# Kernel optimization log

Hardware: AMD Instinct MI355X
Metric: run time of the kernel (lower is better)

The kernel has to match this reference:

```python
import jax, jax.numpy as jnp
import numpy as np

B, N, H = 8, 512, 256
D2 = H // 2          # per-direction hidden = attention proj = 128
VOCAB, EMB = 100, 256
DIN0 = EMB + 3


def _sru_pp_layer(x, pad, Wq, Wk, Wv, Wu, vf, vr, bf, br):
    # x: (L, Bt, din); pad: (L, Bt) bool, True = padded position
    L, Bt, _ = x.shape
    d2 = Wu.shape[1] // 8
    q = x @ Wq                                   # (L,Bt,proj) attention projection
    k = q @ Wk
    v = q @ Wv
    scale = 1.0 / jnp.sqrt(jnp.asarray(q.shape[-1], q.dtype))
    scores = jnp.einsum('lbp,mbp->blm', q, k) * scale
    scores = jnp.where(pad.T[:, None, :], -1e9, scores)
    a = jnp.einsum('blm,mbp->lbp', jax.nn.softmax(scores, axis=-1), v) + q
    U = (a @ Wu).reshape(L, Bt, 2, 4, d2)        # 2 directions x 4 matrices

    def run_dir(Ud, padd, vf_d, vr_d, bf_d, br_d):
        def step(c, inp):
            u, p = inp                            # u: (Bt,4,d2), p: (Bt,)
            f = jax.nn.sigmoid(u[:, 1] + vf_d * c + bf_d)
            r = jax.nn.sigmoid(u[:, 2] + vr_d * c + br_d)
            c_new = f * c + (1.0 - f) * u[:, 0]
            c_new = jnp.where(p[:, None], c, c_new)
            h = jnp.where(p[:, None], 0.0, r * c_new + (1.0 - r) * u[:, 3])
            return c_new, h
        c0 = jnp.zeros((Bt, d2), x.dtype)
        _, hs = jax.lax.scan(step, c0, (Ud, padd))
        return hs

    hf = run_dir(U[:, :, 0], pad, vf[0], vr[0], bf[0], br[0])
    hb = run_dir(U[::-1, :, 1], pad[::-1], vf[1], vr[1], bf[1], br[1])[::-1]
    return jnp.concatenate([hf, hb], axis=-1)     # (L,Bt,2*d2)


def _forward(noisy_seqs, noisy_cords, mask, emb, params):
    Bb, Nn = noisy_seqs.shape
    X = noisy_cords[:, :, 1]                      # CA coordinates (B,N,3)
    m3 = mask[..., None]
    center = (X * m3).sum(1) / m3.sum(1)
    Xc = X - center[:, None] * m3
    C = jnp.einsum('bni,bnj->bij', Xc, Xc)        # (B,3,3) covariance
    _, V = jnp.linalg.eigh(jax.lax.stop_gradient(C))
    ops = jnp.asarray([[i, j, k] for i in (-1, 1) for j in (-1, 1) for k in (-1, 1)], X.dtype)
    F_ops = ops[None, :, None, :] * V[:, None]    # (B,8,3,3) sign-flipped frames
    hX = jnp.einsum('boji,bpj->bopi', F_ops, Xc).reshape(Bb * 8, Nn, 3)
    seq = jnp.where(noisy_seqs < 0, 82, noisy_seqs)
    hS = jnp.broadcast_to(emb[seq][:, None], (Bb, 8, Nn, emb.shape[1])).reshape(Bb * 8, Nn, -1)
    h = jnp.swapaxes(jnp.concatenate([hX, hS], -1), 0, 1)   # (N, B*8, EMB+3)
    pad = jnp.broadcast_to((mask == 0.0)[:, None], (Bb, 8, Nn)).reshape(Bb * 8, Nn).T
    for p in params:
        h = _sru_pp_layer(h, pad, *p)
    return jnp.swapaxes(h, 0, 1).reshape(Bb, 8, Nn, -1).mean(1)


def setup_inputs():
    key = jax.random.key(0)
    ks = [jax.random.fold_in(key, i) for i in range(32)]
    inp = {
        'noisy_seqs': jax.random.randint(ks[0], (B, N), 0, VOCAB, dtype=jnp.int32),
        'noisy_cords': jax.random.normal(ks[1], (B, N, 4, 3), jnp.float32),
        'mask': jnp.ones((B, N), jnp.float32),
        'emb': 0.02 * jax.random.normal(ks[2], (VOCAB, EMB), jnp.float32),
    }
    i = 3
    for l, din in enumerate([DIN0, H]):
        inp[f'Wq{l}'] = jax.random.normal(ks[i], (din, D2), jnp.float32) / np.sqrt(din); i += 1
        inp[f'Wk{l}'] = jax.random.normal(ks[i], (D2, D2), jnp.float32) / np.sqrt(D2); i += 1
        inp[f'Wv{l}'] = jax.random.normal(ks[i], (D2, D2), jnp.float32) / np.sqrt(D2); i += 1
        inp[f'Wu{l}'] = jax.random.normal(ks[i], (D2, 8 * D2), jnp.float32) / np.sqrt(D2); i += 1
        inp[f'vf{l}'] = 0.1 * jax.random.normal(ks[i], (2, D2), jnp.float32); i += 1
        inp[f'vr{l}'] = 0.1 * jax.random.normal(ks[i], (2, D2), jnp.float32); i += 1
        inp[f'bf{l}'] = jnp.zeros((2, D2), jnp.float32)
        inp[f'br{l}'] = jnp.zeros((2, D2), jnp.float32)
    return inp


def reference(noisy_seqs, noisy_cords, mask, emb,
              Wq0, Wk0, Wv0, Wu0, vf0, vr0, bf0, br0,
              Wq1, Wk1, Wv1, Wu1, vf1, vr1, bf1, br1):
    params = [(Wq0, Wk0, Wv0, Wu0, vf0, vr0, bf0, br0),
              (Wq1, Wk1, Wv1, Wu1, vf1, vr1, bf1, br1)]
    return _forward(noisy_seqs, noisy_cords, mask, emb, params)
```

## Files before the change

kernel.cpp:

```cpp
#include <hip/hip_runtime.h>
#include <hip/hip_bf16.h>
#include <math.h>

#define L_    512
#define F_    64
#define M_    (F_*L_)
#define D2_   128
#define H_    256
#define LOG2E_ 1.4426950408889634f

typedef unsigned short u16;
typedef __attribute__((ext_vector_type(8))) short s16x8;
typedef __attribute__((ext_vector_type(4))) float f32x4;

__device__ inline u16 bf_hi(float x) {
  union { float f; unsigned u; } v; v.f = x;
  unsigned r = v.u + 0x7fffu + ((v.u >> 16) & 1u);
  return (u16)(r >> 16);
}
__device__ inline float bf_to_f(u16 h) {
  union { float f; unsigned u; } v; v.u = ((unsigned)h) << 16; return v.f;
}
__device__ inline void split2(float x, u16& h, u16& l) {
  h = bf_hi(x);
  l = bf_hi(x - bf_to_f(h));
}
__device__ inline float exp2_fast(float x) {
#if __has_builtin(__builtin_amdgcn_exp2f)
  return __builtin_amdgcn_exp2f(x);
#else
  return __expf(x * 0.6931471805599453f);
#endif
}
__device__ inline float rcp_fast(float x) {
#if __has_builtin(__builtin_amdgcn_rcpf)
  return __builtin_amdgcn_rcpf(x);
#else
  return 1.f/x;
#endif
}

#define RSPLIT_A 18432
#define RSPLIT_B 26624

__global__ void geom_kernel(const float* __restrict__ cords, const float* __restrict__ mask,
                            float* __restrict__ misc) {
  int b = blockIdx.x;
  int t = threadIdx.x;
  __shared__ float red[4][256];
  float sx=0.f, sy=0.f, sz=0.f, sm=0.f;
  for (int l = t; l < 512; l += 256) {
    float m = mask[b*512 + l];
    const float* X = cords + ((size_t)(b*512 + l)*4 + 1)*3;
    sx += X[0]*m; sy += X[1]*m; sz += X[2]*m; sm += m;
  }
  red[0][t]=sx; red[1][t]=sy; red[2][t]=sz; red[3][t]=sm;
  __syncthreads();
  for (int off=128; off>0; off>>=1) {
    if (t < off) { red[0][t]+=red[0][t+off]; red[1][t]+=red[1][t+off];
                   red[2][t]+=red[2][t+off]; red[3][t]+=red[3][t+off]; }
    __syncthreads();
  }
  float inv = 1.f/red[3][0];
  float cx = red[0][0]*inv, cy = red[1][0]*inv, cz = red[2][0]*inv;
  __syncthreads();
  __shared__ float red6[6][256];
  float c00=0,c01=0,c02=0,c11=0,c12=0,c22=0;
  for (int l = t; l < 512; l += 256) {
    float m = mask[b*512+l];
    const float* X = cords + ((size_t)(b*512+l)*4 + 1)*3;
    float x = X[0]-cx*m, y = X[1]-cy*m, z = X[2]-cz*m;
    c00+=x*x; c01+=x*y; c02+=x*z; c11+=y*y; c12+=y*z; c22+=z*z;
  }
  red6[0][t]=c00; red6[1][t]=c01; red6[2][t]=c02;
  red6[3][t]=c11; red6[4][t]=c12; red6[5][t]=c22;
  __syncthreads();
  for (int off=128; off>0; off>>=1) {
    if (t < off) for (int j=0;j<6;j++) red6[j][t]+=red6[j][t+off];
    __syncthreads();
  }
  if (t == 0) {
    double A[3][3], V[3][3];
    A[0][0]=red6[0][0]; A[0][1]=A[1][0]=red6[1][0]; A[0][2]=A[2][0]=red6[2][0];
    A[1][1]=red6[3][0]; A[1][2]=A[2][1]=red6[4][0]; A[2][2]=red6[5][0];
    for (int j=0;j<3;j++) for (int i=0;i<3;i++) V[j][i] = (i==j)?1.0:0.0;
    for (int sweep=0; sweep<10; ++sweep) {
      for (int p=0;p<2;p++) for (int q=p+1;q<3;q++) {
        double apq = A[p][q];
        if (fabs(apq) < 1e-18) continue;
        double app = A[p][p], aqq = A[q][q];
        double tau = (aqq - app) / (2.0*apq);
        double tt = (tau >= 0.0) ? 1.0/(tau + sqrt(1.0+tau*tau))
                                 : 1.0/(tau - sqrt(1.0+tau*tau));
        double cc = 1.0/sqrt(1.0+tt*tt), ss = tt*cc;
        A[p][p] = app - tt*apq;
        A[q][q] = aqq + tt*apq;
        A[p][q] = A[q][p] = 0.0;
        int r = 3 - p - q;
        double arp = A[r][p], arq = A[r][q];
        A[r][p] = A[p][r] = cc*arp - ss*arq;
        A[r][q] = A[q][r] = ss*arp + cc*arq;
        for (int rr2=0; rr2<3; ++rr2) {
          double vrp = V[rr2][p], vrq = V[rr2][q];
          V[rr2][p] = cc*vrp - ss*vrq;
          V[rr2][q] = ss*vrp + cc*vrq;
        }
      }
    }
    double w[3] = {A[0][0], A[1][1], A[2][2]};
    int idx[3] = {0,1,2};
    for (int i=0;i<2;i++) for (int j=0;j<2-i;j++)
      if (w[idx[j]] > w[idx[j+1]]) { int tmp=idx[j]; idx[j]=idx[j+1]; idx[j+1]=tmp; }
    for (int jj=0;jj<3;jj++) for (int ii=0;ii<3;ii++)
      misc[b*12 + jj*3 + ii] = (float)V[jj][idx[ii]];
    misc[b*12+9]=cx; misc[b*12+10]=cy; misc[b*12+11]=cz;
  }
}

__global__ void build_h0(const int* __restrict__ seqs, const float* __restrict__ cords,
                         const float* __restrict__ mask, const float* __restrict__ emb,
                         const float* __restrict__ misc,
                         u16* __restrict__ h0h, u16* __restrict__ h0l) {
  int t = threadIdx.x;
  int r = blockIdx.x*4 + (t >> 6);
  int lane = t & 63;
  int f = r >> 9, l = r & 511;
  int b = f >> 3, o = f & 7;
  u16* rh = h0h + (size_t)r * 288;
  u16* rl = h0l + (size_t)r * 288;
  if (lane == 0) {
    float m = mask[b*512 + l];
    const float* X = cords + ((size_t)(b*512 + l)*4 + 1)*3;
    const float* mb = misc + b*12;
    float x = X[0]-mb[9]*m, y = X[1]-mb[10]*m, z = X[2]-mb[11]*m;
    #pragma unroll
    for (int i=0;i<3;i++) {
      float sgn = ((o >> (2-i)) & 1) ? 1.f : -1.f;
      float val = sgn * (mb[0+i]*x + mb[3+i]*y + mb[6+i]*z);
      u16 h,lo; split2(val,h,lo); rh[i]=h; rl[i]=lo;
    }
  }
  if (lane < 29) { rh[259+lane] = 0; rl[259+lane] = 0; }
  int s = seqs[b*512 + l];
  if (s < 0) s = 82;
  const float4 e4 = *((const float4*)(emb + (size_t)s*256) + lane);
  float ev[4] = {e4.x, e4.y, e4.z, e4.w};
  #pragma unroll
  for (int i=0;i<4;i++) {
    u16 h,lo; split2(ev[i],h,lo);
    rh[3 + lane*4 + i] = h; rl[3 + lane*4 + i] = lo;
  }
}

__global__ void prep_wqkv_mul(const float* __restrict__ Wq, const float* __restrict__ Wk,
                              const float* __restrict__ Wv,
                              float* __restrict__ wqk, float* __restrict__ wqv) {
  int k = blockIdx.x;
  int y = blockIdx.y;
  int t = threadIdx.x;
  __shared__ float row[128];
  row[t] = Wq[(size_t)k*128 + t];
  __syncthreads();
  const float* W2 = y ? Wv : Wk;
  float acc = 0.f;
  for (int j = 0; j < 128; j++) acc += row[j] * W2[(size_t)j*128 + t];
  (y ? wqv : wqk)[(size_t)k*128 + t] = acc;
}

__global__ void prep_wT3(const float* __restrict__ Wq, const float* __restrict__ wqk,
                         const float* __restrict__ wqv,
                         u16* __restrict__ Th, u16* __restrict__ Tl,
                         int K, int KP) {
  int y = blockIdx.y;
  int n = blockIdx.x;
  const float* W = (y==0) ? Wq : (y==1) ? wqk : wqv;
  int row = y*128 + n;
  for (int k = threadIdx.x; k < KP; k += 128) {
    float x = (k < K) ? W[(size_t)k*128 + n] : 0.f;
    u16 h,l; split2(x,h,l);
    Th[(size_t)row*KP + k] = h; Tl[(size_t)row*KP + k] = l;
  }
}

__global__ void prep_wu(const float* __restrict__ Wu, u16* __restrict__ Th, u16* __restrict__ Tl,
                        const float* __restrict__ bfv, const float* __restrict__ brv,
                        float* __restrict__ nbf, float* __restrict__ nbr) {
  int n = blockIdx.x;
  int dir = blockIdx.y;
  int k = threadIdx.x;
  int d = n >> 2, g = n & 3;
  float x = Wu[(size_t)k*1024 + (dir*4+g)*128 + d];
  if (g == 1 || g == 2) x *= -LOG2E_;
  u16 h,l; split2(x,h,l);
  size_t o = ((size_t)dir*512 + n)*128 + k;
  Th[o]=h; Tl[o]=l;
  if (n == 0) {
    nbf[dir*128 + k] = bfv[dir*128 + k] * (-LOG2E_);
    nbr[dir*128 + k] = brv[dir*128 + k] * (-LOG2E_);
  }
}

template<int EPI>
__global__ __launch_bounds__(256) void gemm_bb(
    const u16* __restrict__ Ah, const u16* __restrict__ Al,
    const u16* __restrict__ Bh, const u16* __restrict__ Bl,
    int KP, int lda, int ldb,
    long aBatch, long bBatch, long cBatch,
    u16* __restrict__ Ch, u16* __restrict__ Cl, int ldc,
    u16* __restrict__ Dh, u16* __restrict__ Dl,
    u16* __restrict__ Eh, u16* __restrict__ El,
    float* __restrict__ F0, float* __restrict__ F1, float* __restrict__ F2,
    float* __restrict__ F3, float* __restrict__ F4, float* __restrict__ F5,
    const u16* __restrict__ rh, const u16* __restrict__ rl,
    const float* __restrict__ maskp, const float* __restrict__ nbf,
    const float* __restrict__ nbr, float scale, int dirOff)
{
  __shared__ u16 As[2][128][40];
  __shared__ u16 Bs[2][128][40];
  __shared__ float epsM[128];
  __shared__ float epsA[128];
  const int t = threadIdx.x;
  const int z = blockIdx.z;
  const int bm = blockIdx.x * 128, bn = blockIdx.y * 128;
  Ah += (size_t)z * aBatch; Al += (size_t)z * aBatch;
  Bh += (size_t)z * bBatch; Bl += (size_t)z * bBatch;

  const int lane = t & 63;
  const int w = t >> 6, wr = w >> 1, wc = w & 1;
  const int fr = lane & 15, g = lane >> 4;

  const bool isD1 = (bn >= 512);
  const int dirU = dirOff + (isD1 ? 1 : 0);
  if (EPI == 4) {
    if (t < 128) {
      int r = bm + t;
      epsM[t] = maskp[(r >> 12)*512 + (r & 511)];
      int nl = (bn + t) & 511;
      int dd = nl >> 2, gg2 = nl & 3;
      epsA[t] = (gg2==1) ? nbf[dirU*128 + dd] : (gg2==2) ? nbr[dirU*128 + dd] : 0.f;
    }
  }

  f32x4 acc[4][4] = {};

  for (int k0 = 0; k0 < KP; k0 += 32) {
    #pragma unroll
    for (int cc = 0; cc < 2; cc++) {
      int c = t + cc*256;
      int m = c >> 2, sub = c & 3;
      const size_t ga = (size_t)(bm + m)*lda + k0 + sub*8;
      const size_t gb = (size_t)(bn + m)*ldb + k0 + sub*8;
      *(int4*)&As[0][m][sub*8] = *(const int4*)(Ah + ga);
      *(int4*)&As[1][m][sub*8] = *(const int4*)(Al + ga);
      *(int4*)&Bs[0][m][sub*8] = *(const int4*)(Bh + gb);
      *(int4*)&Bs[1][m][sub*8] = *(const int4*)(Bl + gb);
    }
    __syncthreads();
    s16x8 af[4][2], bfr[4][2];
    #pragma unroll
    for (int i = 0; i < 4; i++) {
      af[i][0]  = *(const s16x8*)&As[0][wr*64 + i*16 + fr][g*8];
      af[i][1]  = *(const s16x8*)&As[1][wr*64 + i*16 + fr][g*8];
      bfr[i][0] = *(const s16x8*)&Bs[0][wc*64 + i*16 + fr][g*8];
      bfr[i][1] = *(const s16x8*)&Bs[1][wc*64 + i*16 + fr][g*8];
    }
    #pragma unroll
    for (int mi = 0; mi < 4; mi++)
      #pragma unroll
      for (int nj = 0; nj < 4; nj++)
        acc[mi][nj] = __builtin_amdgcn_mfma_f32_16x16x32_bf16(af[mi][0], bfr[nj][0], acc[mi][nj], 0,0,0);
    #pragma unroll
    for (int mi = 0; mi < 4; mi++)
      #pragma unroll
      for (int nj = 0; nj < 4; nj++)
        acc[mi][nj] = __builtin_amdgcn_mfma_f32_16x16x32_bf16(af[mi][0], bfr[nj][1], acc[mi][nj], 0,0,0);
    #pragma unroll
    for (int mi = 0; mi < 4; mi++)
      #pragma unroll
      for (int nj = 0; nj < 4; nj++)
        acc[mi][nj] = __builtin_amdgcn_mfma_f32_16x16x32_bf16(af[mi][1], bfr[nj][0], acc[mi][nj], 0,0,0);
    __syncthreads();
  }

  const int rbase = bm + wr*64, nbase = bn + wc*64;
  float* tA = isD1 ? F3 : F0;
  float* tB = isD1 ? F4 : F1;
  float* tC = isD1 ? F5 : F2;
  const int gg = fr & 3;
  const float ovr = (gg==1) ? -16384.f : (gg==2) ? 16384.f : 0.f;

  #pragma unroll
  for (int mi = 0; mi < 4; mi++) {
    #pragma unroll
    for (int nj = 0; nj < 4; nj++) {
      #pragma unroll
      for (int rg = 0; rg < 4; rg++) {
        int r = rbase + mi*16 + g*4 + rg;
        int n = nbase + nj*16 + fr;
        float val = acc[mi][nj][rg];
        if (EPI == 2) {
          float vv = val * scale;
          if (maskp[(z>>3)*512 + n] == 0.f) vv = -1e9f;
          F0[(size_t)z*cBatch + (size_t)r*ldc + n] = vv;
        } else if (EPI == 3) {
          size_t o = (size_t)z*cBatch + (size_t)r*ldc + n;
          float vv = val + (bf_to_f(rh[o]) + bf_to_f(rl[o]));
          u16 h,l; split2(vv,h,l);
          Ch[o]=h; Cl[o]=l;
        } else if (EPI == 4) {
          int nloc = (n & 511);
          val += epsA[n - bn];
          if (epsM[r - bm] == 0.f) val = ovr;
          float* Up;
          if (r < RSPLIT_A)      Up = tA + (size_t)r*512;
          else if (r < RSPLIT_B) Up = tB + (size_t)(r - RSPLIT_A)*512;
          else                   Up = tC + (size_t)(r - RSPLIT_B)*512;
          Up[nloc] = val;
        } else {
          u16 h,l; split2(val,h,l);
          if (blockIdx.y == 0) {
            size_t o = (size_t)r*128 + n;
            Ch[o]=h; Cl[o]=l;
          } else if (blockIdx.y == 1) {
            size_t o = (size_t)r*128 + (n - 128);
            Dh[o]=h; Dl[o]=l;
          } else {
            size_t o = ((size_t)(r >> 9)*128 + (n - 256))*512 + (r & 511);
            Eh[o]=h; El[o]=l;
          }
        }
      }
    }
  }
}

__global__ __launch_bounds__(256) void attn_flash(
    const u16* __restrict__ qh, const u16* __restrict__ ql,
    const u16* __restrict__ kh, const u16* __restrict__ kl,
    const u16* __restrict__ vTh, const u16* __restrict__ vTl,
    const float* __restrict__ maskp,
    u16* __restrict__ ah, u16* __restrict__ al, float scale)
{
  __shared__ u16 As[2][64][36];
  __shared__ u16 Bs[2][128][36];
  __shared__ u16 Ps[2][64][68];
  __shared__ float rmaxL[2][64];
  __shared__ float rsumL[2][64];
  __shared__ float mskt[64];
  const int t = threadIdx.x;
  const int f = blockIdx.y;
  const int bq = f >> 3;
  const int bm = blockIdx.x * 64;
  const size_t qrow0 = (size_t)f*512 + bm;
  const int lane = t & 63;
  const int w = t >> 6, wr = w >> 1, wc = w & 1;
  const int fr = lane & 15, g = lane >> 4;
  const int m_ = t >> 2, sub_ = t & 3;

  float mrun[2][4], srun[2][4];
  #pragma unroll
  for (int mi=0;mi<2;mi++)
    #pragma unroll
    for (int rg=0;rg<4;rg++) { mrun[mi][rg] = -3e38f; srun[mi][rg] = 0.f; }
  f32x4 Oacc[2][4] = {};

  for (int kt = 0; kt < 8; ++kt) {
    if (t < 64) mskt[t] = maskp[bq*512 + kt*64 + t];
    f32x4 Sacc[2][2] = {};
    #pragma unroll
    for (int k0 = 0; k0 < 4; ++k0) {
      {
        const size_t ga = (qrow0 + m_)*128 + k0*32 + sub_*8;
        const size_t gb = ((size_t)f*512 + kt*64 + m_)*128 + k0*32 + sub_*8;
        *(int4*)&As[0][m_][sub_*8] = *(const int4*)(qh + ga);
        *(int4*)&As[1][m_][sub_*8] = *(const int4*)(ql + ga);
        *(int4*)&Bs[0][m_][sub_*8] = *(const int4*)(kh + gb);
        *(int4*)&Bs[1][m_][sub_*8] = *(const int4*)(kl + gb);
      }
      __syncthreads();
      s16x8 af[2][2], bf2[2][2];
      #pragma unroll
      for (int i = 0; i < 2; i++) {
        af[i][0]  = *(const s16x8*)&As[0][wr*32 + i*16 + fr][g*8];
        af[i][1]  = *(const s16x8*)&As[1][wr*32 + i*16 + fr][g*8];
        bf2[i][0] = *(const s16x8*)&Bs[0][wc*32 + i*16 + fr][g*8];
        bf2[i][1] = *(const s16x8*)&Bs[1][wc*32 + i*16 + fr][g*8];
      }
      #pragma unroll
      for (int mi = 0; mi < 2; mi++)
        #pragma unroll
        for (int nj = 0; nj < 2; nj++)
          Sacc[mi][nj] = __builtin_amdgcn_mfma_f32_16x16x32_bf16(af[mi][0], bf2[nj][0], Sacc[mi][nj], 0,0,0);
      #pragma unroll
      for (int mi = 0; mi < 2; mi++)
        #pragma unroll
        for (int nj = 0; nj < 2; nj++)
          Sacc[mi][nj] = __builtin_amdgcn_mfma_f32_16x16x32_bf16(af[mi][0], bf2[nj][1], Sacc[mi][nj], 0,0,0);
      #pragma unroll
      for (int mi = 0; mi < 2; mi++)
        #pragma unroll
        for (int nj = 0; nj < 2; nj++)
          Sacc[mi][nj] = __builtin_amdgcn_mfma_f32_16x16x32_bf16(af[mi][1], bf2[nj][0], Sacc[mi][nj], 0,0,0);
      __syncthreads();
    }
    float mkv[2];
    mkv[0] = mskt[wc*32 + fr];
    mkv[1] = mskt[wc*32 + 16 + fr];
    float rm[2][4];
    #pragma unroll
    for (int mi=0;mi<2;mi++)
      #pragma unroll
      for (int rg=0;rg<4;rg++) rm[mi][rg] = -3e38f;
    #pragma unroll
    for (int mi=0;mi<2;mi++)
      #pragma unroll
      for (int nj=0;nj<2;nj++)
        #pragma unroll
        for (int rg=0;rg<4;rg++) {
          float sv = Sacc[mi][nj][rg]*scale;
          sv = (mkv[nj]==0.f) ? -1e9f : sv;
          Sacc[mi][nj][rg] = sv;
          rm[mi][rg] = fmaxf(rm[mi][rg], sv);
        }
    #pragma unroll
    for (int off=1; off<16; off<<=1)
      #pragma unroll
      for (int mi=0;mi<2;mi++)
        #pragma unroll
        for (int rg=0;rg<4;rg++) rm[mi][rg] = fmaxf(rm[mi][rg], __shfl_xor(rm[mi][rg], off));
    if (fr == 0) {
      #pragma unroll
      for (int mi=0;mi<2;mi++)
        #pragma unroll
        for (int rg=0;rg<4;rg++) rmaxL[wc][wr*32 + mi*16 + g*4 + rg] = rm[mi][rg];
    }
    __syncthreads();
    float alpha[2][4], rs[2][4];
    #pragma unroll
    for (int mi=0;mi<2;mi++)
      #pragma unroll
      for (int rg=0;rg<4;rg++) {
        int rl_ = wr*32 + mi*16 + g*4 + rg;
        float tmax = fmaxf(rmaxL[0][rl_], rmaxL[1][rl_]);
        float mn = fmaxf(mrun[mi][rg], tmax);
        alpha[mi][rg] = exp2_fast((mrun[mi][rg] - mn)*LOG2E_);
        mrun[mi][rg] = mn;
        rs[mi][rg] = 0.f;
      }
    #pragma unroll
    for (int mi=0;mi<2;mi++)
      #pragma unroll
      for (int nj=0;nj<2;nj++)
        #pragma unroll
        for (int rg=0;rg<4;rg++) {
          float p = exp2_fast((Sacc[mi][nj][rg] - mrun[mi][rg])*LOG2E_);
          rs[mi][rg] += p;
          u16 h,l; split2(p,h,l);
          int rl_ = wr*32 + mi*16 + g*4 + rg;
          int cl_ = wc*32 + nj*16 + fr;
          Ps[0][rl_][cl_] = h;
          Ps[1][rl_][cl_] = l;
        }
    #pragma unroll
    for (int off=1; off<16; off<<=1)
      #pragma unroll
      for (int mi=0;mi<2;mi++)
        #pragma unroll
        for (int rg=0;rg<4;rg++) rs[mi][rg] += __shfl_xor(rs[mi][rg], off);
    if (fr == 0) {
      #pragma unroll
      for (int mi=0;mi<2;mi++)
        #pragma unroll
        for (int rg=0;rg<4;rg++) rsumL[wc][wr*32 + mi*16 + g*4 + rg] = rs[mi][rg];
    }
    #pragma unroll
    for (int mi=0;mi<2;mi++)
      #pragma unroll
      for (int nj=0;nj<4;nj++)
        #pragma unroll
        for (int rg=0;rg<4;rg++) Oacc[mi][nj][rg] *= alpha[mi][rg];
    __syncthreads();
    #pragma unroll
    for (int mi=0;mi<2;mi++)
      #pragma unroll
      for (int rg=0;rg<4;rg++) {
        int rl_ = wr*32 + mi*16 + g*4 + rg;
        srun[mi][rg] = srun[mi][rg]*alpha[mi][rg] + rsumL[0][rl_] + rsumL[1][rl_];
      }
    #pragma unroll
    for (int k0 = 0; k0 < 2; ++k0) {
      #pragma unroll
      for (int cc = 0; cc < 2; cc++) {
        int c = t + cc*256;
        int mv = c >> 2, sb = c & 3;
        const size_t gv = ((size_t)f*128 + mv)*512 + kt*64 + k0*32 + sb*8;
        *(int4*)&Bs[0][mv][sb*8] = *(const int4*)(vTh + gv);
        *(int4*)&Bs[1][mv][sb*8] = *(const int4*)(vTl + gv);
      }
      __syncthreads();
      s16x8 pa[2][2], pb[4][2];
      #pragma unroll
      for (int i = 0; i < 2; i++) {
        pa[i][0] = *(const s16x8*)&Ps[0][wr*32 + i*16 + fr][k0*32 + g*8];
        pa[i][1] = *(const s16x8*)&Ps[1][wr*32 + i*16 + fr][k0*32 + g*8];
      }
      #pragma unroll
      for (int j = 0; j < 4; j++) {
        pb[j][0] = *(const s16x8*)&Bs[0][wc*64 + j*16 + fr][g*8];
        pb[j][1] = *(const s16x8*)&Bs[1][wc*64 + j*16 + fr][g*8];
      }
      #pragma unroll
      for (int mi = 0; mi < 2; mi++)
        #pragma unroll
        for (int nj = 0; nj < 4; nj++)
          Oacc[mi][nj] = __builtin_amdgcn_mfma_f32_16x16x32_bf16(pa[mi][0], pb[nj][0], Oacc[mi][nj], 0,0,0);
      #pragma unroll
      for (int mi = 0; mi < 2; mi++)
        #pragma unroll
        for (int nj = 0; nj < 4; nj++)
          Oacc[mi][nj] = __builtin_amdgcn_mfma_f32_16x16x32_bf16(pa[mi][0], pb[nj][1], Oacc[mi][nj], 0,0,0);
      #pragma unroll
      for (int mi = 0; mi < 2; mi++)
        #pragma unroll
        for (int nj = 0; nj < 4; nj++)
          Oacc[mi][nj] = __builtin_amdgcn_mfma_f32_16x16x32_bf16(pa[mi][1], pb[nj][0], Oacc[mi][nj], 0,0,0);
      __syncthreads();
    }
  }
  float inv[2][4];
  #pragma unroll
  for (int mi=0;mi<2;mi++)
    #pragma unroll
    for (int rg=0;rg<4;rg++) inv[mi][rg] = 1.f / srun[mi][rg];
  #pragma unroll
  for (int mi=0;mi<2;mi++)
    #pragma unroll
    for (int nj=0;nj<4;nj++)
      #pragma unroll
      for (int rg=0;rg<4;rg++) {
        int rl_ = wr*32 + mi*16 + g*4 + rg;
        int cl_ = wc*64 + nj*16 + fr;
        size_t o = (qrow0 + rl_)*128 + cl_;
        float val = Oacc[mi][nj][rg]*inv[mi][rg] + bf_to_f(qh[o]) + bf_to_f(ql[o]);
        u16 h,l; split2(val,h,l);
        ah[o]=h; al[o]=l;
      }
}

__global__ void softmax_split(float* __restrict__ S) {
  size_t row = blockIdx.x;
  float* p = S + row*512;
  u16* ph = (u16*)p;
  u16* pl = ph + 512;
  int t = threadIdx.x;
  float v[8];
  float mx = -1e30f;
  #pragma unroll
  for (int i=0;i<8;i++) { v[i] = p[t + i*64]; mx = fmaxf(mx, v[i]); }
  #pragma unroll
  for (int off=32; off>0; off>>=1) mx = fmaxf(mx, __shfl_xor(mx, off));
  float sum = 0.f;
  #pragma unroll
  for (int i=0;i<8;i++) { v[i] = __expf(v[i]-mx); sum += v[i]; }
  #pragma unroll
  for (int off=32; off>0; off>>=1) sum += __shfl_xor(sum, off);
  float invs = 1.f/sum;
  #pragma unroll
  for (int i=0;i<8;i++) {
    float x = v[i]*invs;
    u16 h,l; split2(x,h,l);
    ph[t + i*64] = h; pl[t + i*64] = l;
  }
}

#define CH_ 8
#define LOADC(buf, ch) do { \
  int _c = (ch); \
  _Pragma("unroll") \
  for (int s = 0; s < CH_; s++) { \
    int l = (_c*CH_ + s) ^ lxor; \
    buf[s] = *(const float4*)(Ubase + (size_t)l*512); \
  } \
  __builtin_amdgcn_sched_barrier(0); \
} while(0)

#define COMPC(buf, ch) do { \
  int _c = (ch); \
  _Pragma("unroll") \
  for (int s = 0; s < CH_; s++) { \
    int l = (_c*CH_ + s) ^ lxor; \
    float4 u = buf[s]; \
    float ef = exp2_fast(fmaf(nvfd, cstate, u.y)); \
    float fg = rcp_fast(1.f + ef); \
    float er = exp2_fast(fmaf(nvrd, cstate, u.z)); \
    float rg = rcp_fast(1.f + er); \
    float cn = fmaf(fg, cstate - u.x, u.x); \
    float h  = fmaf(rg, cn - u.w, u.w); \
    cstate = cn; \
    if (PAIRS) { \
      u16 sh_, sl_; split2(h, sh_, sl_); \
      hpph[(size_t)l*256] = sh_; \
      hppl[(size_t)l*256] = sl_; \
    } else { \
      h32p[(size_t)l*256] = h; \
    } \
  } \
  __builtin_amdgcn_sched_barrier(0); \
} while(0)

template<int PAIRS>
__global__ __launch_bounds__(64, 1) void sru_scan(
                          const float* __restrict__ ua0, const float* __restrict__ ub0,
                          const float* __restrict__ uc0,
                          const float* __restrict__ ua1, const float* __restrict__ ub1,
                          const float* __restrict__ uc1,
                          const float* __restrict__ vf, const float* __restrict__ vr,
                          u16* __restrict__ hph, u16* __restrict__ hpl,
                          float* __restrict__ h32, int dirArg) {
  const int blk = blockIdx.x;
  const int f = blk >> 1;
  const int hh = blk & 1;
  const int dir = dirArg + blockIdx.y;
  const int t = threadIdx.x;
  const int lxor = dir ? 511 : 0;
  const int d = hh*64 + t;
  const float nvfd = vf[dir*128 + d] * (-LOG2E_);
  const float nvrd = vr[dir*128 + d] * (-LOG2E_);
  const size_t fbase = (size_t)f * 512;
  const float* ua = dir ? ua1 : ua0;
  const float* ub = dir ? ub1 : ub0;
  const float* uc = dir ? uc1 : uc0;
  const float* Uf;
  if (f < 36)      Uf = ua + (size_t)f*(512*512);
  else if (f < 52) Uf = ub + (size_t)(f-36)*(512*512);
  else             Uf = uc + (size_t)(f-52)*(512*512);
  const float* Ubase = Uf + d*4;
  u16* hpph = hph + fbase*256 + (size_t)dir*128 + d;
  u16* hppl = hpl + fbase*256 + (size_t)dir*128 + d;
  float* h32p = h32 + fbase*256 + (size_t)dir*128 + d;

  float4 b0[CH_], b1[CH_], b2[CH_], b3[CH_];
  LOADC(b0, 0); LOADC(b1, 1);
  float cstate = 0.f;
  #pragma unroll 1
  for (int q4 = 0; q4 < 15; q4++) {
    const int base = q4*4;
    LOADC(b2, base+2);
    COMPC(b0, base);
    LOADC(b3, base+3);
    COMPC(b1, base+1);
    LOADC(b0, base+4);
    COMPC(b2, base+2);
    LOADC(b1, base+5);
    COMPC(b3, base+3);
  }
  LOADC(b2, 62);
  COMPC(b0, 60);
  LOADC(b3, 63);
  COMPC(b1, 61);
  COMPC(b2, 62);
  COMPC(b3, 63);
}

__global__ void mean_kernel(const float* __restrict__ h2, float* __restrict__ out) {
  int i = blockIdx.x*256 + threadIdx.x;
  int row = i >> 6;
  int c4  = i & 63;
  int b = row >> 9, l = row & 511;
  float ax=0.f, ay=0.f, az=0.f, aw=0.f;
  #pragma unroll
  for (int o=0;o<8;o++) {
    const float4* p = (const float4*)(h2 + ((size_t)((b*8+o)*512 + l))*256) + c4;
    float4 e = *p;
    ax += e.x; ay += e.y; az += e.z; aw += e.w;
  }
  float4 r; r.x = ax*0.125f; r.y = ay*0.125f; r.z = az*0.125f; r.w = aw*0.125f;
  ((float4*)out)[i] = r;
}

extern "C" void kernel_launch(void* const* d_in, const int* in_sizes, int n_in,
                              void* d_out, int out_size, void* d_ws, size_t ws_size,
                              hipStream_t stream) {
  const int*   seqs  = (const int*)d_in[0];
  const float* cords = (const float*)d_in[1];
  const float* mask  = (const float*)d_in[2];
  const float* emb   = (const float*)d_in[3];
  const float* Wq[2] = {(const float*)d_in[4],  (const float*)d_in[12]};
  const float* Wk[2] = {(const float*)d_in[5],  (const float*)d_in[13]};
  const float* Wv[2] = {(const float*)d_in[6],  (const float*)d_in[14]};
  const float* Wu[2] = {(const float*)d_in[7],  (const float*)d_in[15]};
  const float* vf[2] = {(const float*)d_in[8],  (const float*)d_in[16]};
  const float* vr[2] = {(const float*)d_in[9],  (const float*)d_in[17]};
  const float* bfp[2]= {(const float*)d_in[10], (const float*)d_in[18]};
  const float* brp[2]= {(const float*)d_in[11], (const float*)d_in[19]};

  const size_t H0_B = 2*(size_t)M_*288*2;
  const size_t Q_B  = 2*(size_t)M_*128*2;
  const size_t S_B  = (size_t)M_*512*4;
  const size_t HP_B = 2*(size_t)M_*256*2;
  const size_t W_B  = (size_t)(2*1024*128)*2 + 2*256*4;

  const size_t NEED_MERGED = 4096 + H0_B + 3*Q_B + S_B + HP_B + W_B;
  const bool merged = (ws_size >= NEED_MERGED);

  char* base = (char*)d_ws;
  float* misc = (float*)base;
  u16* h0p_h = (u16*)(base + 4096);
  u16* h0p_l = h0p_h + (size_t)M_*288;
  u16* q_h   = (u16*)(base + 4096 + H0_B);
  u16* q_l   = q_h + (size_t)M_*128;
  u16* k_h   = (u16*)(base + 4096 + H0_B + Q_B);
  u16* k_l   = k_h + (size_t)M_*128;

  u16 *vT_h, *vT_l, *a_h, *a_l;
  float *S, *tail_w;
  u16 *hp_h, *hp_l;
  float *U1A, *U1B, *U1C;
  if (merged) {
    vT_h = (u16*)(base + 4096 + H0_B + 2*Q_B);
    vT_l = vT_h + (size_t)M_*128;
    S    = (float*)(base + 4096 + H0_B + 3*Q_B);
    hp_h = (u16*)((char*)S + S_B);
    hp_l = hp_h + (size_t)M_*256;
    tail_w = (float*)((char*)hp_h + HP_B);
    U1A = (float*)h0p_h;
    U1B = (float*)q_h;
    U1C = (float*)vT_h;
    a_h = hp_h;
    a_l = hp_h + (size_t)M_*128;
  } else {
    S    = (float*)(base + 4096 + H0_B + 2*Q_B);
    hp_h = (u16*)((char*)S + S_B);
    hp_l = hp_h + (size_t)M_*256;
    vT_h = hp_h; vT_l = hp_l;
    tail_w = (float*)((char*)hp_h + HP_B);
    U1A = S; U1B = S + (size_t)RSPLIT_A*512; U1C = S + (size_t)RSPLIT_B*512;
    a_h = k_h; a_l = k_l;
  }
  float* U0A = S;
  float* U0B = S + (size_t)RSPLIT_A*512;
  float* U0C = S + (size_t)RSPLIT_B*512;
  float* h32 = (float*)hp_h;

  float* wqk32 = S;
  float* wqv32 = wqk32 + 288*128;
  u16*   wT3h  = (u16*)(wqv32 + 288*128);
  u16*   wT3l  = wT3h + 384*288;
  u16* wuT_h = (u16*)tail_w;
  u16* wuT_l = wuT_h + 1024*128;
  float* nbf = (float*)(wuT_l + 1024*128);
  float* nbr = nbf + 256;

  geom_kernel<<<8, 256, 0, stream>>>(cords, mask, misc);
  build_h0<<<M_/4, 256, 0, stream>>>(seqs, cords, mask, emb, misc, h0p_h, h0p_l);

  const float scale = 0.08838834764831845f;
  for (int layer = 0; layer < 2; ++layer) {
    const u16* Ah_in = layer ? hp_h : h0p_h;
    const u16* Al_in = layer ? hp_l : h0p_l;
    const int  Kq    = layer ? 256 : 259;
    const int  KPq   = layer ? 256 : 288;

    prep_wqkv_mul<<<dim3(Kq,2), 128, 0, stream>>>(Wq[layer], Wk[layer], Wv[layer], wqk32, wqv32);
    prep_wT3<<<dim3(128,3), 128, 0, stream>>>(Wq[layer], wqk32, wqv32, wT3h, wT3l, Kq, KPq);
    prep_wu<<<dim3(512,2), 128, 0, stream>>>(Wu[layer], wuT_h, wuT_l, bfp[layer], brp[layer], nbf, nbr);

    gemm_bb<5><<<dim3(256,3,1), 256, 0, stream>>>(Ah_in, Al_in, wT3h, wT3l,
        KPq, KPq, KPq, 0,0,0, q_h, q_l, 128, k_h, k_l, vT_h, vT_l,
        nullptr,nullptr,nullptr,nullptr,nullptr,nullptr,
        nullptr,nullptr, nullptr,nullptr,nullptr, 0.f, 0);

    if (merged) {
      attn_flash<<<dim3(8,64), 256, 0, stream>>>(q_h, q_l, k_h, k_l, vT_h, vT_l,
          mask, a_h, a_l, scale);
    } else {
      gemm_bb<2><<<dim3(4,4,64), 256, 0, stream>>>(q_h, q_l, k_h, k_l,
          128, 128, 128, 512*128, 512*128, 512*512, nullptr,nullptr, 512,
          nullptr,nullptr,nullptr,nullptr,
          S,nullptr,nullptr,nullptr,nullptr,nullptr,
          nullptr,nullptr, mask,nullptr,nullptr, scale, 0);
      softmax_split<<<M_, 64, 0, stream>>>(S);
      gemm_bb<3><<<dim3(4,1,64), 256, 0, stream>>>((const u16*)S, (const u16*)S + 512, vT_h, vT_l,
          512, 1024, 512, 512*1024, 128*512, 512*128, a_h, a_l, 128,
          nullptr,nullptr,nullptr,nullptr,
          nullptr,nullptr,nullptr,nullptr,nullptr,nullptr,
          q_h, q_l, nullptr,nullptr,nullptr, 0.f, 0);
    }

    if (merged) {
      gemm_bb<4><<<dim3(256,8,1), 256, 0, stream>>>(a_h, a_l, wuT_h, wuT_l,
          128, 128, 128, 0,0,0, nullptr,nullptr, 512,
          nullptr,nullptr,nullptr,nullptr,
          U0A,U0B,U0C, U1A,U1B,U1C,
          nullptr,nullptr, mask, nbf, nbr, 0.f, 0);
      if (layer == 0)
        sru_scan<1><<<dim3(128,2), 64, 0, stream>>>(U0A,U0B,U0C, U1A,U1B,U1C,
            vf[layer], vr[layer], hp_h, hp_l, h32, 0);
      else
        sru_scan<0><<<dim3(128,2), 64, 0, stream>>>(U0A,U0B,U0C, U1A,U1B,U1C,
            vf[layer], vr[layer], hp_h, hp_l, h32, 0);
    } else {
      for (int dir = 0; dir < 2; ++dir) {
        gemm_bb<4><<<dim3(256,4,1), 256, 0, stream>>>(a_h, a_l,
            wuT_h + (size_t)dir*512*128, wuT_l + (size_t)dir*512*128,
            128, 128, 128, 0,0,0, nullptr,nullptr, 512,
            nullptr,nullptr,nullptr,nullptr,
            U0A,U0B,U0C, U0A,U0B,U0C,
            nullptr,nullptr, mask, nbf, nbr, 0.f, dir);
        if (layer == 0)
          sru_scan<1><<<dim3(128,1), 64, 0, stream>>>(U0A,U0B,U0C, U0A,U0B,U0C,
              vf[layer], vr[layer], hp_h, hp_l, h32, dir);
        else
          sru_scan<0><<<dim3(128,1), 64, 0, stream>>>(U0A,U0B,U0C, U0A,U0B,U0C,
              vf[layer], vr[layer], hp_h, hp_l, h32, dir);
      }
    }
  }
  mean_kernel<<<1024, 256, 0, stream>>>(h32, (float*)d_out);
}
```

Baseline: 468.4 us.

## Fuse U projection GEMM into SRU scan kernel via LDS-staged chunks

Replaces the separate U-projection GEMM (which wrote the full fp32 U tensor to global memory) and the following SRU scan with a single fused kernel. Each block computes 64-timestep chunks of U for its sequence, direction and channel half with MFMA, stages them in about 120KB of LDS, then one wavefront runs the recurrence over the chunk. This removes the large U global write and read. In exchange only 64 of 256 threads do the serial scan while the others idle, and the grid has just 256 blocks at one block per CU.

```diff
diff --git a/kernel.cpp b/kernel.cpp
--- a/kernel.cpp
+++ b/kernel.cpp
@@ -39,9 +39,6 @@
   return 1.f/x;
 #endif
 }
-
-#define RSPLIT_A 18432
-#define RSPLIT_B 26624
 
 __global__ void geom_kernel(const float* __restrict__ cords, const float* __restrict__ mask,
                             float* __restrict__ misc) {
@@ -209,16 +206,12 @@
     u16* __restrict__ Ch, u16* __restrict__ Cl, int ldc,
     u16* __restrict__ Dh, u16* __restrict__ Dl,
     u16* __restrict__ Eh, u16* __restrict__ El,
-    float* __restrict__ F0, float* __restrict__ F1, float* __restrict__ F2,
-    float* __restrict__ F3, float* __restrict__ F4, float* __restrict__ F5,
+    float* __restrict__ F0,
     const u16* __restrict__ rh, const u16* __restrict__ rl,
-    const float* __restrict__ maskp, const float* __restrict__ nbf,
-    const float* __restrict__ nbr, float scale, int dirOff)
+    const float* __restrict__ maskp, float scale)
 {
   __shared__ u16 As[2][128][40];
   __shared__ u16 Bs[2][128][40];
-  __shared__ float epsM[128];
-  __shared__ float epsA[128];
   const int t = threadIdx.x;
   const int z = blockIdx.z;
   const int bm = blockIdx.x * 128, bn = blockIdx.y * 128;
@@ -228,18 +221,6 @@
   const int lane = t & 63;
   const int w = t >> 6, wr = w >> 1, wc = w & 1;
   const int fr = lane & 15, g = lane >> 4;
-
-  const bool isD1 = (bn >= 512);
-  const int dirU = dirOff + (isD1 ? 1 : 0);
-  if (EPI == 4) {
-    if (t < 128) {
-      int r = bm + t;
-      epsM[t] = maskp[(r >> 12)*512 + (r & 511)];
-      int nl = (bn + t) & 511;
-      int dd = nl >> 2, gg2 = nl & 3;
-      epsA[t] = (gg2==1) ? nbf[dirU*128 + dd] : (gg2==2) ? nbr[dirU*128 + dd] : 0.f;
-    }
-  }
 
   f32x4 acc[4][4] = {};
 
@@ -283,12 +264,6 @@
   }
 
   const int rbase = bm + wr*64, nbase = bn + wc*64;
-  float* tA = isD1 ? F3 : F0;
-  float* tB = isD1 ? F4 : F1;
-  float* tC = isD1 ? F5 : F2;
-  const int gg = fr & 3;
-  const float ovr = (gg==1) ? -16384.f : (gg==2) ? 16384.f : 0.f;
-
   #pragma unroll
   for (int mi = 0; mi < 4; mi++) {
     #pragma unroll
@@ -307,15 +282,6 @@
           float vv = val + (bf_to_f(rh[o]) + bf_to_f(rl[o]));
           u16 h,l; split2(vv,h,l);
           Ch[o]=h; Cl[o]=l;
-        } else if (EPI == 4) {
-          int nloc = (n & 511);
-          val += epsA[n - bn];
-          if (epsM[r - bm] == 0.f) val = ovr;
-          float* Up;
-          if (r < RSPLIT_A)      Up = tA + (size_t)r*512;
-          else if (r < RSPLIT_B) Up = tB + (size_t)(r - RSPLIT_A)*512;
-          else                   Up = tC + (size_t)(r - RSPLIT_B)*512;
-          Up[nloc] = val;
         } else {
           u16 h,l; split2(val,h,l);
           if (blockIdx.y == 0) {
@@ -573,93 +539,138 @@
   }
 }
 
-#define CH_ 8
-#define LOADC(buf, ch) do { \
-  int _c = (ch); \
-  _Pragma("unroll") \
-  for (int s = 0; s < CH_; s++) { \
-    int l = (_c*CH_ + s) ^ lxor; \
-    buf[s] = *(const float4*)(Ubase + (size_t)l*512); \
-  } \
-  __builtin_amdgcn_sched_barrier(0); \
-} while(0)
-
-#define COMPC(buf, ch) do { \
-  int _c = (ch); \
-  _Pragma("unroll") \
-  for (int s = 0; s < CH_; s++) { \
-    int l = (_c*CH_ + s) ^ lxor; \
-    float4 u = buf[s]; \
-    float ef = exp2_fast(fmaf(nvfd, cstate, u.y)); \
-    float fg = rcp_fast(1.f + ef); \
-    float er = exp2_fast(fmaf(nvrd, cstate, u.z)); \
-    float rg = rcp_fast(1.f + er); \
-    float cn = fmaf(fg, cstate - u.x, u.x); \
-    float h  = fmaf(rg, cn - u.w, u.w); \
-    cstate = cn; \
-    if (PAIRS) { \
-      u16 sh_, sl_; split2(h, sh_, sl_); \
-      hpph[(size_t)l*256] = sh_; \
-      hppl[(size_t)l*256] = sl_; \
-    } else { \
-      h32p[(size_t)l*256] = h; \
-    } \
-  } \
-  __builtin_amdgcn_sched_barrier(0); \
-} while(0)
-
+#define SRU_LDS_BYTES 122176
 template<int PAIRS>
-__global__ __launch_bounds__(64, 1) void sru_scan(
-                          const float* __restrict__ ua0, const float* __restrict__ ub0,
-                          const float* __restrict__ uc0,
-                          const float* __restrict__ ua1, const float* __restrict__ ub1,
-                          const float* __restrict__ uc1,
-                          const float* __restrict__ vf, const float* __restrict__ vr,
-                          u16* __restrict__ hph, u16* __restrict__ hpl,
-                          float* __restrict__ h32, int dirArg) {
-  const int blk = blockIdx.x;
-  const int f = blk >> 1;
-  const int hh = blk & 1;
-  const int dir = dirArg + blockIdx.y;
+__global__ __launch_bounds__(256, 1) void sru_fused(
+    const u16* __restrict__ Ah, const u16* __restrict__ Al,
+    const u16* __restrict__ wuTh, const u16* __restrict__ wuTl,
+    const float* __restrict__ maskp,
+    const float* __restrict__ nbf, const float* __restrict__ nbr,
+    const float* __restrict__ vf, const float* __restrict__ vr,
+    u16* __restrict__ hph, u16* __restrict__ hpl, float* __restrict__ h32)
+{
+  extern __shared__ char smem[];
+  float* Uc   = (float*)smem;
+  u16*   As   = (u16*)(smem + 69696);
+  u16*   Bs   = (u16*)(smem + 69696 + 10240);
+  float* epsA = (float*)(smem + 120896);
+  float* mskc = (float*)(smem + 121920);
+  const int UPL = 4356;
+
+  const int f = blockIdx.x, dir = blockIdx.y, hh = blockIdx.z;
   const int t = threadIdx.x;
-  const int lxor = dir ? 511 : 0;
-  const int d = hh*64 + t;
-  const float nvfd = vf[dir*128 + d] * (-LOG2E_);
-  const float nvrd = vr[dir*128 + d] * (-LOG2E_);
-  const size_t fbase = (size_t)f * 512;
-  const float* ua = dir ? ua1 : ua0;
-  const float* ub = dir ? ub1 : ub0;
-  const float* uc = dir ? uc1 : uc0;
-  const float* Uf;
-  if (f < 36)      Uf = ua + (size_t)f*(512*512);
-  else if (f < 52) Uf = ub + (size_t)(f-36)*(512*512);
-  else             Uf = uc + (size_t)(f-52)*(512*512);
-  const float* Ubase = Uf + d*4;
-  u16* hpph = hph + fbase*256 + (size_t)dir*128 + d;
-  u16* hppl = hpl + fbase*256 + (size_t)dir*128 + d;
-  float* h32p = h32 + fbase*256 + (size_t)dir*128 + d;
-
-  float4 b0[CH_], b1[CH_], b2[CH_], b3[CH_];
-  LOADC(b0, 0); LOADC(b1, 1);
+  const int lane = t & 63, w = t >> 6;
+  const int fr = lane & 15, g = lane >> 4;
+  const int b = f >> 3;
+
+  {
+    int gate = t & 3, dl = t >> 2;
+    int ch = dir*128 + hh*64 + dl;
+    epsA[t] = (gate==1) ? nbf[ch] : (gate==2) ? nbr[ch] : 0.f;
+  }
+  const float nvfd = vf[dir*128 + hh*64 + lane] * (-LOG2E_);
+  const float nvrd = vr[dir*128 + hh*64 + lane] * (-LOG2E_);
+  const int chx = dir ? 7 : 0, lx = dir ? 63 : 0;
+  const int gate = fr & 3;
+  const float ovr = (gate==1) ? -16384.f : (gate==2) ? 16384.f : 0.f;
   float cstate = 0.f;
+
   #pragma unroll 1
-  for (int q4 = 0; q4 < 15; q4++) {
-    const int base = q4*4;
-    LOADC(b2, base+2);
-    COMPC(b0, base);
-    LOADC(b3, base+3);
-    COMPC(b1, base+1);
-    LOADC(b0, base+4);
-    COMPC(b2, base+2);
-    LOADC(b1, base+5);
-    COMPC(b3, base+3);
-  }
-  LOADC(b2, 62);
-  COMPC(b0, 60);
-  LOADC(b3, 63);
-  COMPC(b1, 61);
-  COMPC(b2, 62);
-  COMPC(b3, 63);
+  for (int ci = 0; ci < 8; ++ci) {
+    const int ch = ci ^ chx;
+    if (t < 64) mskc[t] = maskp[b*512 + ch*64 + t];
+    f32x4 acc[4][4] = {};
+    #pragma unroll 1
+    for (int k0 = 0; k0 < 4; ++k0) {
+      {
+        int m = t >> 2, sub = t & 3;
+        size_t ga = ((size_t)f*512 + ch*64 + m)*128 + k0*32 + sub*8;
+        *(int4*)&As[(0*64 + m)*40 + sub*8] = *(const int4*)(Ah + ga);
+        *(int4*)&As[(1*64 + m)*40 + sub*8] = *(const int4*)(Al + ga);
+      }
+      {
+        size_t gb = ((size_t)(dir*512 + hh*256 + t))*128 + k0*32;
+        #pragma unroll
+        for (int s4 = 0; s4 < 4; ++s4) {
+          *(int4*)&Bs[(0*256 + t)*40 + s4*8] = *(const int4*)(wuTh + gb + s4*8);
+          *(int4*)&Bs[(1*256 + t)*40 + s4*8] = *(const int4*)(wuTl + gb + s4*8);
+        }
+      }
+      __syncthreads();
+      s16x8 af[4][2], bfr[4][2];
+      #pragma unroll
+      for (int i = 0; i < 4; i++) {
+        af[i][0]  = *(const s16x8*)&As[(0*64 + i*16 + fr)*40 + g*8];
+        af[i][1]  = *(const s16x8*)&As[(1*64 + i*16 + fr)*40 + g*8];
+        bfr[i][0] = *(const s16x8*)&Bs[(0*256 + w*64 + i*16 + fr)*40 + g*8];
+        bfr[i][1] = *(const s16x8*)&Bs[(1*256 + w*64 + i*16 + fr)*40 + g*8];
+      }
+      #pragma unroll
+      for (int mi = 0; mi < 4; mi++)
+        #pragma unroll
+        for (int nj = 0; nj < 4; nj++)
+          acc[mi][nj] = __builtin_amdgcn_mfma_f32_16x16x32_bf16(af[mi][0], bfr[nj][0], acc[mi][nj], 0,0,0);
+      #pragma unroll
+      for (int mi = 0; mi < 4; mi++)
+        #pragma unroll
+        for (int nj = 0; nj < 4; nj++)
+          acc[mi][nj] = __builtin_amdgcn_mfma_f32_16x16x32_bf16(af[mi][0], bfr[nj][1], acc[mi][nj], 0,0,0);
+      #pragma unroll
+      for (int mi = 0; mi < 4; mi++)
+        #pragma unroll
+        for (int nj = 0; nj < 4; nj++)
+          acc[mi][nj] = __builtin_amdgcn_mfma_f32_16x16x32_bf16(af[mi][1], bfr[nj][0], acc[mi][nj], 0,0,0);
+      __syncthreads();
+    }
+    #pragma unroll
+    for (int mi = 0; mi < 4; mi++) {
+      #pragma unroll
+      for (int nj = 0; nj < 4; nj++) {
+        int nl = w*64 + nj*16 + fr;
+        int dl = nl >> 2;
+        float ea = epsA[nl];
+        #pragma unroll
+        for (int rg = 0; rg < 4; rg++) {
+          int r = mi*16 + g*4 + rg;
+          float val = acc[mi][nj][rg] + ea;
+          if (mskc[r] == 0.f) val = ovr;
+          Uc[gate*UPL + r*68 + dl] = val;
+        }
+      }
+    }
+    __syncthreads();
+    if (t < 64) {
+      const int d = t;
+      int l0 = 0 ^ lx, l1 = 1 ^ lx;
+      float a0 = Uc[0*UPL + l0*68 + d], a1 = Uc[1*UPL + l0*68 + d];
+      float a2 = Uc[2*UPL + l0*68 + d], a3 = Uc[3*UPL + l0*68 + d];
+      float b0 = Uc[0*UPL + l1*68 + d], b1 = Uc[1*UPL + l1*68 + d];
+      float b2 = Uc[2*UPL + l1*68 + d], b3 = Uc[3*UPL + l1*68 + d];
+      #pragma unroll 4
+      for (int si = 0; si < 64; ++si) {
+        float n0=0.f, n1=0.f, n2=0.f, n3=0.f;
+        if (si + 2 < 64) {
+          int ln = (si+2) ^ lx;
+          n0 = Uc[0*UPL + ln*68 + d]; n1 = Uc[1*UPL + ln*68 + d];
+          n2 = Uc[2*UPL + ln*68 + d]; n3 = Uc[3*UPL + ln*68 + d];
+        }
+        float ef = exp2_fast(fmaf(nvfd, cstate, a1));
+        float fg = rcp_fast(1.f + ef);
+        float er = exp2_fast(fmaf(nvrd, cstate, a2));
+        float rg2 = rcp_fast(1.f + er);
+        float cn = fmaf(fg, cstate - a0, a0);
+        float h  = fmaf(rg2, cn - a3, a3);
+        cstate = cn;
+        int ll = si ^ lx;
+        size_t o = ((size_t)f*512 + ch*64 + ll)*256 + dir*128 + hh*64 + d;
+        if (PAIRS) { u16 sh_, sl_; split2(h, sh_, sl_); hph[o]=sh_; hpl[o]=sl_; }
+        else h32[o] = h;
+        a0=b0; a1=b1; a2=b2; a3=b3;
+        b0=n0; b1=n1; b2=n2; b3=n3;
+      }
+    }
+    __syncthreads();
+  }
 }
 
 __global__ void mean_kernel(const float* __restrict__ h2, float* __restrict__ out) {
@@ -715,7 +726,6 @@
   u16 *vT_h, *vT_l, *a_h, *a_l;
   float *S, *tail_w;
   u16 *hp_h, *hp_l;
-  float *U1A, *U1B, *U1C;
   if (merged) {
     vT_h = (u16*)(base + 4096 + H0_B + 2*Q_B);
     vT_l = vT_h + (size_t)M_*128;
@@ -723,23 +733,16 @@
     hp_h = (u16*)((char*)S + S_B);
     hp_l = hp_h + (size_t)M_*256;
     tail_w = (float*)((char*)hp_h + HP_B);
-    U1A = (float*)h0p_h;
-    U1B = (float*)q_h;
-    U1C = (float*)vT_h;
-    a_h = hp_h;
-    a_l = hp_h + (size_t)M_*128;
+    a_h = (u16*)S;
+    a_l = a_h + (size_t)M_*128;
   } else {
     S    = (float*)(base + 4096 + H0_B + 2*Q_B);
     hp_h = (u16*)((char*)S + S_B);
     hp_l = hp_h + (size_t)M_*256;
     vT_h = hp_h; vT_l = hp_l;
     tail_w = (float*)((char*)hp_h + HP_B);
-    U1A = S; U1B = S + (size_t)RSPLIT_A*512; U1C = S + (size_t)RSPLIT_B*512;
     a_h = k_h; a_l = k_l;
   }
-  float* U0A = S;
-  float* U0B = S + (size_t)RSPLIT_A*512;
-  float* U0C = S + (size_t)RSPLIT_B*512;
   float* h32 = (float*)hp_h;
 
   float* wqk32 = S;
@@ -767,8 +770,7 @@
 
     gemm_bb<5><<<dim3(256,3,1), 256, 0, stream>>>(Ah_in, Al_in, wT3h, wT3l,
         KPq, KPq, KPq, 0,0,0, q_h, q_l, 128, k_h, k_l, vT_h, vT_l,
-        nullptr,nullptr,nullptr,nullptr,nullptr,nullptr,
-        nullptr,nullptr, nullptr,nullptr,nullptr, 0.f, 0);
+        nullptr, nullptr,nullptr, nullptr, 0.f);
 
     if (merged) {
       attn_flash<<<dim3(8,64), 256, 0, stream>>>(q_h, q_l, k_h, k_l, vT_h, vT_l,
@@ -777,44 +779,20 @@
       gemm_bb<2><<<dim3(4,4,64), 256, 0, stream>>>(q_h, q_l, k_h, k_l,
           128, 128, 128, 512*128, 512*128, 512*512, nullptr,nullptr, 512,
           nullptr,nullptr,nullptr,nullptr,
-          S,nullptr,nullptr,nullptr,nullptr,nullptr,
-          nullptr,nullptr, mask,nullptr,nullptr, scale, 0);
+          S, nullptr,nullptr, mask, scale);
       softmax_split<<<M_, 64, 0, stream>>>(S);
       gemm_bb<3><<<dim3(4,1,64), 256, 0, stream>>>((const u16*)S, (const u16*)S + 512, vT_h, vT_l,
           512, 1024, 512, 512*1024, 128*512, 512*128, a_h, a_l, 128,
           nullptr,nullptr,nullptr,nullptr,
-          nullptr,nullptr,nullptr,nullptr,nullptr,nullptr,
-          q_h, q_l, nullptr,nullptr,nullptr, 0.f, 0);
-    }
-
-    if (merged) {
-      gemm_bb<4><<<dim3(256,8,1), 256, 0, stream>>>(a_h, a_l, wuT_h, wuT_l,
-          128, 128, 128, 0,0,0, nullptr,nullptr, 512,
-          nullptr,nullptr,nullptr,nullptr,
-          U0A,U0B,U0C, U1A,U1B,U1C,
-          nullptr,nullptr, mask, nbf, nbr, 0.f, 0);
-      if (layer == 0)
-        sru_scan<1><<<dim3(128,2), 64, 0, stream>>>(U0A,U0B,U0C, U1A,U1B,U1C,
-            vf[layer], vr[layer], hp_h, hp_l, h32, 0);
-      else
-        sru_scan<0><<<dim3(128,2), 64, 0, stream>>>(U0A,U0B,U0C, U1A,U1B,U1C,
-            vf[layer], vr[layer], hp_h, hp_l, h32, 0);
-    } else {
-      for (int dir = 0; dir < 2; ++dir) {
-        gemm_bb<4><<<dim3(256,4,1), 256, 0, stream>>>(a_h, a_l,
-            wuT_h + (size_t)dir*512*128, wuT_l + (size_t)dir*512*128,
-            128, 128, 128, 0,0,0, nullptr,nullptr, 512,
-            nullptr,nullptr,nullptr,nullptr,
-            U0A,U0B,U0C, U0A,U0B,U0C,
-            nullptr,nullptr, mask, nbf, nbr, 0.f, dir);
-        if (layer == 0)
-          sru_scan<1><<<dim3(128,1), 64, 0, stream>>>(U0A,U0B,U0C, U0A,U0B,U0C,
-              vf[layer], vr[layer], hp_h, hp_l, h32, dir);
-        else
-          sru_scan<0><<<dim3(128,1), 64, 0, stream>>>(U0A,U0B,U0C, U0A,U0B,U0C,
-              vf[layer], vr[layer], hp_h, hp_l, h32, dir);
-      }
-    }
+          nullptr, q_h, q_l, nullptr, 0.f);
+    }
+
+    if (layer == 0)
+      sru_fused<1><<<dim3(64,2,2), 256, SRU_LDS_BYTES, stream>>>(a_h, a_l,
+          wuT_h, wuT_l, mask, nbf, nbr, vf[layer], vr[layer], hp_h, hp_l, h32);
+    else
+      sru_fused<0><<<dim3(64,2,2), 256, SRU_LDS_BYTES, stream>>>(a_h, a_l,
+          wuT_h, wuT_l, mask, nbf, nbr, vf[layer], vr[layer], hp_h, hp_l, h32);
   }
   mean_kernel<<<1024, 256, 0, stream>>>(h32, (float*)d_out);
 }
```

Measured after the change: 527.8 us. 1.13x slower.
